# Kernel optimization log

Measured on AMD Instinct MI355X. Metric: run time of the kernel, lower is better.

The kernel has to match this reference:

```python
import jax, jax.numpy as jnp
import numpy as np

EPS_TOTAL = 1e-6
EPS_LOG = 1e-7


def setup_inputs() -> dict:
    key = jax.random.key(0)
    k1, k2 = jax.random.split(key)
    z = jax.random.normal(k1, (16, 4096, 64), dtype=jnp.float32)
    codebook = jax.random.normal(k2, (1024, 64), dtype=jnp.float32)
    return {"z": z, "codebook": codebook}


def reference(z, codebook):
    # z: [B, T, C]; codebook: [K, C]. Eval-mode forward (mask=None).
    B, T, C = z.shape
    K = codebook.shape[0]
    x = z.reshape(-1, C)  # [N, C]

    # quantize: squared-distance matrix via matmul + argmin (fp32 math)
    d = ((x * x).sum(-1, keepdims=True)
         - 2.0 * (x @ codebook.T)
         + (codebook * codebook).sum(-1)[None, :])  # [N, K]
    code_idx = jnp.argmin(d, axis=-1)  # [N]

    # dequantize: gather codewords
    z_q = codebook[code_idx]  # [N, C]

    # commitment loss: MSE to detached codewords, mean over tokens
    per_tok = ((x - jax.lax.stop_gradient(z_q)) ** 2).mean(-1)  # [N]
    commit_loss = per_tok.mean()

    # straight-through estimator
    z_q_bar = x + jax.lax.stop_gradient(z_q - x)

    # compute_perplexity metrics (eval path): one-hot scatter histogram
    counts = jnp.zeros((K,), dtype=x.dtype).at[code_idx].add(1.0)
    total = jnp.maximum(counts.sum(), EPS_TOTAL)
    prob = counts / total
    ppl = jnp.exp(-(prob * jnp.log(prob + EPS_LOG)).sum())
    usage = (counts >= 1.0).astype(x.dtype).mean()

    return z_q_bar.reshape(B, T, C), commit_loss, ppl, usage
```

## Files before the change

### kernel.cpp

```cpp
#include <hip/hip_runtime.h>


typedef _Float16 half8 __attribute__((ext_vector_type(8)));
typedef float f32x4 __attribute__((ext_vector_type(4)));

#define NTOK 65536
#define KCODE 1024
#define OUT_SCALARS 4194304
#define MARGIN 1e-3f

#define WS_CNT   1024
#define WS_LOSS  2048
#define WS_CBHL  20480

static __device__ __forceinline__ unsigned int order_key(float f) {
    unsigned int u = __float_as_uint(f);
    unsigned int mask = (u >> 31) ? 0xFFFFFFFFu : 0x80000000u;
    return u ^ mask;
}
static __device__ __forceinline__ float key_to_float(unsigned int k) {
    unsigned int u = (k & 0x80000000u) ? (k ^ 0x80000000u) : ~k;
    return __uint_as_float(u);
}
static __device__ __forceinline__ unsigned long long umin64(unsigned long long a,
                                                            unsigned long long b) {
    return a < b ? a : b;
}
static __device__ __forceinline__ unsigned long long umax64(unsigned long long a,
                                                            unsigned long long b) {
    return a > b ? a : b;
}

__global__ void prep_kernel(const float* __restrict__ cb, float* __restrict__ ws) {
    const int k = blockIdx.x * 256 + threadIdx.x;
    const float4* cb4 = (const float4*)cb;
    float s = 0.f;
#pragma unroll
    for (int j = 0; j < 16; ++j) {
        float4 v = cb4[k * 16 + j];
        s = fmaf(v.x, v.x, s);
        s = fmaf(v.y, v.y, s);
        s = fmaf(v.z, v.z, s);
        s = fmaf(v.w, v.w, s);
    }
    ws[k] = s;
    ws[WS_CNT + k] = 0.f;

    _Float16* base = (_Float16*)(ws + WS_CBHL) + (size_t)(k >> 4) * 2048 + (k & 15) * 64;
    const int c = k & 15;
#pragma unroll
    for (int d8 = 0; d8 < 8; ++d8) {
        float4 a = cb4[k * 16 + 2 * d8], b = cb4[k * 16 + 2 * d8 + 1];
        float xf[8] = {a.x, a.y, a.z, a.w, b.x, b.y, b.z, b.w};
        half8 h, lo;
#pragma unroll
        for (int i = 0; i < 8; ++i) {
            _Float16 hi = (_Float16)xf[i];
            h[i] = hi;
            lo[i] = (_Float16)((xf[i] - (float)hi) * 4096.f);
        }
        const int pos = ((d8 + c) & 7) * 8;
        *(half8*)(base + pos) = h;
        *(half8*)(base + 1024 + pos) = lo;
    }
}

__launch_bounds__(256, 4)
__global__ void quant_kernel(const float* __restrict__ z,
                             const float* __restrict__ cb,
                             float* __restrict__ out,
                             float* __restrict__ ws) {
    const int t = threadIdx.x, blk = blockIdx.x;
    const int w = t >> 6, l = t & 63;
    const int cl = l & 15, g = l >> 4;
    const int tok0 = blk * 64;
    const int tokL = w * 16 + cl;
    const int tokG = tok0 + tokL;

    __shared__ __align__(16) _Float16 tiles[4][2][2048];
    __shared__ __align__(16) float cn_lds[1024];
    __shared__ int win[64];
    __shared__ float lsum[64];

    *(float4*)&cn_lds[t * 4] = *(const float4*)(ws + t * 4);

    half8 zh[2], zl[2];
    {
        const float4* z4 = (const float4*)z + (size_t)tokG * 16;
#pragma unroll
        for (int q = 0; q < 2; ++q) {
            float4 a = z4[2 * g + 8 * q], b = z4[2 * g + 8 * q + 1];
            float xf[8] = {a.x, a.y, a.z, a.w, b.x, b.y, b.z, b.w};
#pragma unroll
            for (int i = 0; i < 8; ++i) {
                _Float16 h = (_Float16)xf[i];
                zh[q][i] = h;
                zl[q][i] = (_Float16)((xf[i] - (float)h) * 4096.f);
            }
        }
    }

    asm volatile("s_waitcnt vmcnt(0) lgkmcnt(0)" ::: "memory");
    __builtin_amdgcn_sched_barrier(0);

    const char* dma_src = (const char*)(ws + WS_CBHL) + w * 1024 + l * 16;
    const int rot = (g + cl) & 7;
    const int o0 = cl * 64 + rot * 8;
    const int o1 = cl * 64 + (rot ^ 4) * 8;

#pragma unroll
    for (int p = 0; p < 3; ++p)
#pragma unroll
        for (int u = 0; u < 2; ++u)
            __builtin_amdgcn_global_load_lds(
                (const __attribute__((address_space(1))) void*)(dma_src + (p * 2 + u) * 4096),
                (__attribute__((address_space(3))) void*)&tiles[p][u][w * 512], 16, 0, 0);

    float d1 = 3.4e38f, d2 = 3.4e38f;
    int idx1 = 0, idx2 = 0;

#define TILE_COMPUTE(ti, TP)                                                          \
    {                                                                                 \
        const _Float16* tp = (TP);                                                    \
        half8 H0 = *(const half8*)(tp + o0);                                          \
        half8 H1 = *(const half8*)(tp + o1);                                          \
        half8 L0 = *(const half8*)(tp + 1024 + o0);                                   \
        half8 L1 = *(const half8*)(tp + 1024 + o1);                                   \
        float4 cnv = *(const float4*)&cn_lds[(ti) * 16 + 4 * g];                      \
        const float cna[4] = {cnv.x, cnv.y, cnv.z, cnv.w};                            \
        f32x4 a1 = {0.f,0.f,0.f,0.f}, a2 = {0.f,0.f,0.f,0.f};                         \
        a1 = __builtin_amdgcn_mfma_f32_16x16x32_f16(H0, zh[0], a1, 0, 0, 0);          \
        a1 = __builtin_amdgcn_mfma_f32_16x16x32_f16(H1, zh[1], a1, 0, 0, 0);          \
        a2 = __builtin_amdgcn_mfma_f32_16x16x32_f16(H0, zl[0], a2, 0, 0, 0);          \
        a2 = __builtin_amdgcn_mfma_f32_16x16x32_f16(H1, zl[1], a2, 0, 0, 0);          \
        a2 = __builtin_amdgcn_mfma_f32_16x16x32_f16(L0, zh[0], a2, 0, 0, 0);          \
        a2 = __builtin_amdgcn_mfma_f32_16x16x32_f16(L1, zh[1], a2, 0, 0, 0);          \
        _Pragma("unroll")                                                             \
        for (int r = 0; r < 4; ++r) {                                                 \
            float dot = fmaf(a2[r], 2.44140625e-4f, a1[r]);                           \
            float d = fmaf(-2.f, dot, cna[r]);                                        \
            const int kidx = (ti) * 16 + 4 * g + r;                                   \
            bool lt = d < d1;                                                         \
            bool mid = d < d2;                                                        \
            idx2 = lt ? idx1 : (mid ? kidx : idx2);    \
            d2 = fminf(d2, fmaxf(d, d1));                                             \
            idx1 = lt ? kidx : idx1;                                                  \
            d1 = fminf(d1, d);                                                        \
        }                                                                             \
    }

#define PHASE(P, SLOT, SLOT2, VM, ISSUE)                                              \
    {                                                                                 \
        asm volatile("s_waitcnt vmcnt(" VM ")" ::: "memory");                         \
        asm volatile("s_barrier" ::: "memory");                                       \
        if (ISSUE) {                                                                  \
            _Pragma("unroll")                                                         \
            for (int u = 0; u < 2; ++u)                                               \
                __builtin_amdgcn_global_load_lds(                                     \
                    (const __attribute__((address_space(1))) void*)(dma_src + (((P) + 3) * 2 + u) * 4096), \
                    (__attribute__((address_space(3))) void*)&tiles[SLOT2][u][w * 512], \
                    16, 0, 0);                                                        \
        }                                                                             \
        TILE_COMPUTE((P) * 2 + 0, &tiles[SLOT][0][0])                                 \
        TILE_COMPUTE((P) * 2 + 1, &tiles[SLOT][1][0])                                 \
    }

    for (int i4 = 0; i4 < 28; i4 += 4) {
        PHASE(i4 + 0, 0, 3, "4", 1)
        PHASE(i4 + 1, 1, 0, "4", 1)
        PHASE(i4 + 2, 2, 1, "4", 1)
        PHASE(i4 + 3, 3, 2, "4", 1)
    }
    PHASE(28, 0, 3, "4", 1)
    PHASE(29, 1, 0, "4", 0)
    PHASE(30, 2, 0, "2", 0)
    PHASE(31, 3, 0, "0", 0)
#undef PHASE
#undef TILE_COMPUTE

    unsigned long long k1 = ((unsigned long long)order_key(d1) << 32) | (unsigned)idx1;
    unsigned long long k2 = ((unsigned long long)order_key(d2) << 32) | (unsigned)idx2;
#pragma unroll
    for (int off = 16; off <= 32; off <<= 1) {
        unsigned long long ok1 = __shfl_xor(k1, off, 64);
        unsigned long long ok2 = __shfl_xor(k2, off, 64);
        unsigned long long lo = umin64(k1, ok1);
        unsigned long long hi = umax64(k1, ok1);
        k2 = umin64(hi, umin64(k2, ok2));
        k1 = lo;
    }

    if (l < 16) {
        int fidx = (int)(unsigned)(k1 & 0xFFFFFFFFull);
        const float d1f = key_to_float((unsigned)(k1 >> 32));
        const float d2f = key_to_float((unsigned)(k2 >> 32));
        if (d2f - d1f < MARGIN) {
            const int ia = fidx;
            const int ib = (int)(unsigned)(k2 & 0xFFFFFFFFull);
            const float4* zr = (const float4*)z + (size_t)tokG * 16;
            const float4* ca = (const float4*)cb + (size_t)ia * 16;
            const float4* cbp = (const float4*)cb + (size_t)ib * 16;
            float sa = 0.f, sb = 0.f;
#pragma unroll
            for (int j = 0; j < 16; ++j) {
                float4 xv = zr[j];
                float4 va = ca[j], vb = cbp[j];
                sa = fmaf(xv.x, va.x, sa); sb = fmaf(xv.x, vb.x, sb);
                sa = fmaf(xv.y, va.y, sa); sb = fmaf(xv.y, vb.y, sb);
                sa = fmaf(xv.z, va.z, sa); sb = fmaf(xv.z, vb.z, sb);
                sa = fmaf(xv.w, va.w, sa); sb = fmaf(xv.w, vb.w, sb);
            }
            const float ea = fmaf(-2.f, sa, cn_lds[ia]);
            const float eb = fmaf(-2.f, sb, cn_lds[ib]);
            const unsigned long long ka = ((unsigned long long)order_key(ea) << 32) | (unsigned)ia;
            const unsigned long long kb = ((unsigned long long)order_key(eb) << 32) | (unsigned)ib;
            fidx = (int)(unsigned)(umin64(ka, kb) & 0xFFFFFFFFull);
        }
        win[tokL] = fidx;
        atomicAdd(&ws[WS_CNT + fidx], 1.f);
    }
    __syncthreads();

    {
        const int tokr = t >> 2, fb = (t & 3) * 4;
        const int idx = win[tokr];
        const float4* zr = (const float4*)z + (size_t)(tok0 + tokr) * 16;
        const float4* cq = (const float4*)cb + (size_t)idx * 16;
        float4* o4 = (float4*)out + (size_t)(tok0 + tokr) * 16;
        float ss = 0.f;
#pragma unroll
        for (int j = 0; j < 4; ++j) {
            float4 xv = zr[fb + j];
            float4 qv = cq[fb + j];
            float4 ov; float dx;
            dx = qv.x - xv.x; ov.x = xv.x + dx; ss = fmaf(dx, dx, ss);
            dx = qv.y - xv.y; ov.y = xv.y + dx; ss = fmaf(dx, dx, ss);
            dx = qv.z - xv.z; ov.z = xv.z + dx; ss = fmaf(dx, dx, ss);
            dx = qv.w - xv.w; ov.w = xv.w + dx; ss = fmaf(dx, dx, ss);
            o4[fb + j] = ov;
        }
        ss += __shfl_down(ss, 2, 64);
        ss += __shfl_down(ss, 1, 64);
        if ((t & 3) == 0) lsum[tokr] = ss * (1.f / 64.f);
    }
    __syncthreads();
    if (t < 64) {
        float v = lsum[t];
#pragma unroll
        for (int off = 32; off > 0; off >>= 1) v += __shfl_down(v, off, 64);
        if (t == 0) ws[WS_LOSS + blk] = v;
    }
}

__global__ void final_kernel(const float* __restrict__ ws, float* __restrict__ out) {
    const int t = threadIdx.x;
    const int l = t & 63, wv = t >> 6;
    __shared__ float rbuf[16];

#define BLOCK_REDUCE(VAR, EXPR)                                             \
    float VAR;                                                              \
    {                                                                       \
        float v_ = (EXPR);                                                  \
        _Pragma("unroll")                                                   \
        for (int off = 32; off > 0; off >>= 1) v_ += __shfl_down(v_, off, 64); \
        if (l == 0) rbuf[wv] = v_;                                          \
        __syncthreads();                                                    \
        float r_ = (t < 16) ? rbuf[t] : 0.f;                                \
        if (wv == 0) {                                                      \
            _Pragma("unroll")                                               \
            for (int off = 8; off > 0; off >>= 1) r_ += __shfl_down(r_, off, 64); \
            if (l == 0) rbuf[0] = r_;                                       \
        }                                                                   \
        __syncthreads();                                                    \
        VAR = rbuf[0];                                                      \
        __syncthreads();                                                    \
    }

    const float c = ws[WS_CNT + t];
    BLOCK_REDUCE(totraw, c)
    const float total = fmaxf(totraw, 1e-6f);
    const float p = c / total;
    BLOCK_REDUCE(ent, p * logf(p + 1e-7f))
    BLOCK_REDUCE(used, (c >= 1.f) ? 1.f : 0.f)
    BLOCK_REDUCE(loss, ws[WS_LOSS + t])
#undef BLOCK_REDUCE

    if (t == 0) {
        out[OUT_SCALARS + 0] = loss * (1.f / (float)NTOK);
        out[OUT_SCALARS + 1] = expf(-ent);
        out[OUT_SCALARS + 2] = used * (1.f / (float)KCODE);
    }
}

extern "C" void kernel_launch(void* const* d_in, const int* in_sizes, int n_in,
                              void* d_out, int out_size, void* d_ws, size_t ws_size,
                              hipStream_t stream) {
    const float* z  = (const float*)d_in[0];
    const float* cb = (const float*)d_in[1];
    float* out = (float*)d_out;
    float* ws  = (float*)d_ws;

    prep_kernel <<<4, 256, 0, stream>>>(cb, ws);
    quant_kernel<<<NTOK / 64, 256, 0, stream>>>(z, cb, out, ws);
    final_kernel<<<1, 1024, 0, stream>>>(ws, out);
}
```

Baseline: 82.78 us.

## Replace block-shared codebook tiles with per-wave private ring buffers without barriers

Each wave now streams the full codebook tile (hi and lo halves) into its own 3-slot LDS ring instead of the four waves cooperatively loading a shared 4-slot buffer, and the per-phase s_barrier is removed in favour of per-wave vmcnt waits. This removes block-wide synchronisation stalls between waves in the main distance loop. In exchange each wave issues four times as many global-to-LDS loads for the same data. LDS use grows from 32KB to 48KB of tiles, so launch bounds drop from 4 to 3 blocks per CU, reducing occupancy.

```diff
diff --git a/kernel.cpp b/kernel.cpp
--- a/kernel.cpp
+++ b/kernel.cpp
@@ -65,7 +65,7 @@
     }
 }
 
-__launch_bounds__(256, 4)
+__launch_bounds__(256, 3)
 __global__ void quant_kernel(const float* __restrict__ z,
                              const float* __restrict__ cb,
                              float* __restrict__ out,
@@ -77,7 +77,7 @@
     const int tokL = w * 16 + cl;
     const int tokG = tok0 + tokL;
 
-    __shared__ __align__(16) _Float16 tiles[4][2][2048];
+    __shared__ __align__(16) _Float16 ring[4][3][2048];
     __shared__ __align__(16) float cn_lds[1024];
     __shared__ int win[64];
     __shared__ float lsum[64];
@@ -102,32 +102,42 @@
 
     asm volatile("s_waitcnt vmcnt(0) lgkmcnt(0)" ::: "memory");
     __builtin_amdgcn_sched_barrier(0);
-
-    const char* dma_src = (const char*)(ws + WS_CBHL) + w * 1024 + l * 16;
+    __syncthreads();
+
+    const char* dma_src = (const char*)(ws + WS_CBHL) + l * 16;
     const int rot = (g + cl) & 7;
     const int o0 = cl * 64 + rot * 8;
     const int o1 = cl * 64 + (rot ^ 4) * 8;
 
 #pragma unroll
-    for (int p = 0; p < 3; ++p)
-#pragma unroll
-        for (int u = 0; u < 2; ++u)
+    for (int p = 0; p < 2; ++p)
+#pragma unroll
+        for (int q = 0; q < 4; ++q)
             __builtin_amdgcn_global_load_lds(
-                (const __attribute__((address_space(1))) void*)(dma_src + (p * 2 + u) * 4096),
-                (__attribute__((address_space(3))) void*)&tiles[p][u][w * 512], 16, 0, 0);
+                (const __attribute__((address_space(1))) void*)(dma_src + p * 4096 + q * 1024),
+                (__attribute__((address_space(3))) void*)&ring[w][p][q * 512], 16, 0, 0);
 
     float d1 = 3.4e38f, d2 = 3.4e38f;
     int idx1 = 0, idx2 = 0;
 
-#define TILE_COMPUTE(ti, TP)                                                          \
+#define TILE_BODY(ti, SLOT, VM, ISSUE)                                                \
     {                                                                                 \
-        const _Float16* tp = (TP);                                                    \
+        asm volatile("s_waitcnt vmcnt(" VM ")" ::: "memory");                         \
+        const _Float16* tp = &ring[w][SLOT][0];                                       \
         half8 H0 = *(const half8*)(tp + o0);                                          \
         half8 H1 = *(const half8*)(tp + o1);                                          \
         half8 L0 = *(const half8*)(tp + 1024 + o0);                                   \
         half8 L1 = *(const half8*)(tp + 1024 + o1);                                   \
         float4 cnv = *(const float4*)&cn_lds[(ti) * 16 + 4 * g];                      \
         const float cna[4] = {cnv.x, cnv.y, cnv.z, cnv.w};                            \
+        if (ISSUE) {                                                                  \
+            _Pragma("unroll")                                                         \
+            for (int q = 0; q < 4; ++q)                                               \
+                __builtin_amdgcn_global_load_lds(                                     \
+                    (const __attribute__((address_space(1))) void*)(dma_src + ((ti) + 2) * 4096 + q * 1024), \
+                    (__attribute__((address_space(3))) void*)&ring[w][((SLOT) + 2) % 3][q * 512], \
+                    16, 0, 0);                                                        \
+        }                                                                             \
         f32x4 a1 = {0.f,0.f,0.f,0.f}, a2 = {0.f,0.f,0.f,0.f};                         \
         a1 = __builtin_amdgcn_mfma_f32_16x16x32_f16(H0, zh[0], a1, 0, 0, 0);          \
         a1 = __builtin_amdgcn_mfma_f32_16x16x32_f16(H1, zh[1], a1, 0, 0, 0);          \
@@ -149,34 +159,16 @@
         }                                                                             \
     }
 
-#define PHASE(P, SLOT, SLOT2, VM, ISSUE)                                              \
-    {                                                                                 \
-        asm volatile("s_waitcnt vmcnt(" VM ")" ::: "memory");                         \
-        asm volatile("s_barrier" ::: "memory");                                       \
-        if (ISSUE) {                                                                  \
-            _Pragma("unroll")                                                         \
-            for (int u = 0; u < 2; ++u)                                               \
-                __builtin_amdgcn_global_load_lds(                                     \
-                    (const __attribute__((address_space(1))) void*)(dma_src + (((P) + 3) * 2 + u) * 4096), \
-                    (__attribute__((address_space(3))) void*)&tiles[SLOT2][u][w * 512], \
-                    16, 0, 0);                                                        \
-        }                                                                             \
-        TILE_COMPUTE((P) * 2 + 0, &tiles[SLOT][0][0])                                 \
-        TILE_COMPUTE((P) * 2 + 1, &tiles[SLOT][1][0])                                 \
-    }
-
-    for (int i4 = 0; i4 < 28; i4 += 4) {
-        PHASE(i4 + 0, 0, 3, "4", 1)
-        PHASE(i4 + 1, 1, 0, "4", 1)
-        PHASE(i4 + 2, 2, 1, "4", 1)
-        PHASE(i4 + 3, 3, 2, "4", 1)
-    }
-    PHASE(28, 0, 3, "4", 1)
-    PHASE(29, 1, 0, "4", 0)
-    PHASE(30, 2, 0, "2", 0)
-    PHASE(31, 3, 0, "0", 0)
-#undef PHASE
-#undef TILE_COMPUTE
+    for (int i3 = 0; i3 < 60; i3 += 3) {
+        TILE_BODY(i3 + 0, 0, "4", 1)
+        TILE_BODY(i3 + 1, 1, "4", 1)
+        TILE_BODY(i3 + 2, 2, "4", 1)
+    }
+    TILE_BODY(60, 0, "4", 1)
+    TILE_BODY(61, 1, "4", 1)
+    TILE_BODY(62, 2, "4", 0)
+    TILE_BODY(63, 0, "0", 0)
+#undef TILE_BODY
 
     unsigned long long k1 = ((unsigned long long)order_key(d1) << 32) | (unsigned)idx1;
     unsigned long long k2 = ((unsigned long long)order_key(d2) << 32) | (unsigned)idx2;
```

Result: faster. 80.31 us, median of 2 (-3.0%).
